# Optimization experiments

Measured on AMD Instinct MI355X. Metric: run time of the kernel, lower is better.

Reference implementation:

```python
import jax, jax.numpy as jnp
import numpy as np

G = 3040      # number of drugs / graph nodes in the drug-drug graph
A = 100       # atoms per molecular graph (smileNode, uniform)
TOK = 43      # token vocabulary (hard-coded in module)
FS = 75       # nfeat_smile
HS = 128      # nhid_smile
H1S = 128     # nhid1_smile
NF = 512      # nfeat (raw 384 + 128 smile emb)
NH = 256      # nhid
DH = 256      # dhid1


def setup_inputs() -> dict:
    key = jax.random.key(0)
    ks = jax.random.split(key, 20)
    s = 0.05
    inp = {
        "x": jax.random.normal(ks[0], (G, NF - H1S), dtype=jnp.float32),
        "adj_pos": jax.random.uniform(ks[1], (G, G), dtype=jnp.float32) / G,
        "adj_neg": jax.random.uniform(ks[2], (G, G), dtype=jnp.float32) / G,
        "mol_adj": jax.random.uniform(ks[3], (G, A, A), dtype=jnp.float32) / A,
        "encoded_drug": jax.random.randint(ks[4], (G, A), 0, TOK, dtype=jnp.int64),
        # learned params
        "tok_emb": jax.random.normal(ks[5], (TOK, FS), dtype=jnp.float32),
        "Wm1": jax.random.normal(ks[6], (G, FS, HS), dtype=jnp.float32) * s,
        "Wm2": jax.random.normal(ks[7], (G, HS, H1S), dtype=jnp.float32) * s,
        "Wp1": jax.random.normal(ks[8], (NF, NH), dtype=jnp.float32) * s,
        "Wp2": jax.random.normal(ks[9], (NH, NH), dtype=jnp.float32) * s,
        "Wn1": jax.random.normal(ks[10], (NF, NH), dtype=jnp.float32) * s,
        "Wn2": jax.random.normal(ks[11], (NH, NH), dtype=jnp.float32) * s,
        "Wd1": jax.random.normal(ks[12], (2 * NH, DH), dtype=jnp.float32) * s,
        "Wd2": jax.random.normal(ks[13], (DH, 2 * DH), dtype=jnp.float32) * s,
        "Wd3": jax.random.normal(ks[14], (2 * DH, DH), dtype=jnp.float32) * s,
        "Wdec": jax.random.normal(ks[15], (DH, DH), dtype=jnp.float32) * s,
    }
    return inp


def reference(x, adj_pos, adj_neg, mol_adj, encoded_drug, tok_emb,
              Wm1, Wm2, Wp1, Wp2, Wn1, Wn2, Wd1, Wd2, Wd3, Wdec):
    # --- calDrugSmileFeatures: batched over all 3040 per-graph GCN encoders ---
    feats = tok_emb[encoded_drug]                          # [G, A, FS] (embedding gather)
    h = jnp.einsum('gab,gaf,gfh->gbh', mol_adj, feats, Wm1)  # gc1: adj @ (x @ W1), per graph
    h = jnp.einsum('gab,gah,ghk->gbk', mol_adj, h, Wm2)      # gc2 (dropout inactive, eval)
    emb_drugs = jnp.max(h, axis=1)                          # [G, H1S] node-wise maxpool

    # --- main drug-drug graph ---
    xc = jnp.concatenate([x, emb_drugs], axis=1)            # [G, NF]
    hp = jax.nn.relu(adj_pos @ (xc @ Wp1))                  # GCNEncoder pos layer1
    zp = adj_pos @ (hp @ Wp2)                               # layer2
    hn = jax.nn.relu(adj_neg @ (xc @ Wn1))
    zn = adj_neg @ (hn @ Wn2)
    z = jnp.concatenate([zp, zn], axis=1)                   # [G, 2*NH]

    # --- DSN MLP (eval: dropout inactive) ---
    z = jax.nn.relu(z @ Wd1)
    z = jax.nn.relu(z @ Wd2)
    z = z @ Wd3                                             # [G, DH]

    # --- Bilinear decoder: z W z^T logits ---
    y_pred = (z @ Wdec) @ z.T                               # [G, G]
    return y_pred
```

## Files before the change

kernel.cpp:

```cpp
#include <hip/hip_runtime.h>
#include <cstdint>
#include <cstddef>

#define Gn   3040
#define An   100
#define TOKn 43
#define FSn  75
#define NFn  512
#define XC   384

typedef __attribute__((ext_vector_type(8))) short s16x8;
typedef __attribute__((ext_vector_type(4))) float f32x4;

__device__ __forceinline__ void split_bf16(float x, unsigned short &h, unsigned short &l)
{
  unsigned u = __float_as_uint(x);
  unsigned r = (u + 0x7fffu + ((u >> 16) & 1u)) & 0xffff0000u;
  h = (unsigned short)(r >> 16);
  float res = x - __uint_as_float(r);
  unsigned v = __float_as_uint(res);
  l = (unsigned short)((v + 0x7fffu + ((v >> 16) & 1u)) >> 16);
}

#define MFMA3(acc, ah, al, bh, bl)                                              \
  acc = __builtin_amdgcn_mfma_f32_16x16x32_bf16(ah, bh, acc, 0, 0, 0);          \
  acc = __builtin_amdgcn_mfma_f32_16x16x32_bf16(ah, bl, acc, 0, 0, 0);          \
  acc = __builtin_amdgcn_mfma_f32_16x16x32_bf16(al, bh, acc, 0, 0, 0);

__device__ __forceinline__ s16x8 tail_frag(const unsigned short* p, bool act)
{
  s16x8 f = {0,0,0,0,0,0,0,0};
  if (act) {
    uint2 v = *(const uint2*)p;
    f[0] = (short)(v.x & 0xffffu); f[1] = (short)(v.x >> 16);
    f[2] = (short)(v.y & 0xffffu); f[3] = (short)(v.y >> 16);
  }
  return f;
}

__device__ __forceinline__ void pack_split4(const f32x4 a, uint2 &ph, uint2 &pl)
{
  unsigned short h[4], l[4];
  #pragma unroll
  for (int r = 0; r < 4; ++r) split_bf16(a[r], h[r], l[r]);
  ph.x = (unsigned)h[0] | ((unsigned)h[1] << 16);
  ph.y = (unsigned)h[2] | ((unsigned)h[3] << 16);
  pl.x = (unsigned)l[0] | ((unsigned)l[1] << 16);
  pl.y = (unsigned)l[2] | ((unsigned)l[3] << 16);
}

__global__ void prep_tok_kernel(const float* __restrict__ tok_emb,
                                unsigned short* __restrict__ th,
                                unsigned short* __restrict__ tl)
{
  int i = blockIdx.x * 256 + threadIdx.x;
  if (i >= TOKn * 96) return;
  int r = i / 96, f = i % 96;
  float v = (f < FSn) ? tok_emb[r * FSn + f] : 0.f;
  unsigned short h, l;
  split_bf16(v, h, l);
  th[i] = h; tl[i] = l;
}

__global__ __launch_bounds__(512, 1) void smile_mfma_kernel(
    const float* __restrict__ mol_adj, const int* __restrict__ enc,
    const unsigned short* __restrict__ tokh, const unsigned short* __restrict__ tokl,
    const float* __restrict__ Wm1, const float* __restrict__ Wm2,
    float* __restrict__ xc)
{
  __shared__ __align__(16) unsigned short sm[74624];
  unsigned short* adjT_h = sm;
  unsigned short* adjT_l = sm + 10400;
  unsigned short* bufA_h = sm + 20800;
  unsigned short* bufA_l = sm + 34112;
  unsigned short* g1_h   = sm + 47424;
  unsigned short* g1_l   = sm + 61024;
  float* Sf = (float*)(sm + 20800);

  const int g = blockIdx.x;
  const int t = threadIdx.x;
  const int w = t >> 6, l = t & 63;
  const int lr = l & 15, lq = l >> 4;
  const f32x4 z4 = {0.f, 0.f, 0.f, 0.f};
  const s16x8 z8 = {0,0,0,0,0,0,0,0};

  const float* adjg = mol_adj + (size_t)g * (An * An);
  float4 av[5];
  #pragma unroll
  for (int j = 0; j < 5; ++j) {
    const int i = t + 512 * j;
    av[j] = make_float4(0.f, 0.f, 0.f, 0.f);
    if (i < 2500) av[j] = *(const float4*)&adjg[i * 4];
  }
  const int hcol = 16 * w + lr;
  const float* W1 = Wm1 + (size_t)g * (FSn * 128);
  float w1r[3][8];
  #pragma unroll
  for (int kc = 0; kc < 3; ++kc)
    #pragma unroll
    for (int j = 0; j < 8; ++j) {
      const int f = 32 * kc + 8 * lq + j;
      w1r[kc][j] = (f < FSn) ? W1[f * 128 + hcol] : 0.f;
    }
  const float* W2 = Wm2 + (size_t)g * (128 * 128);
  float w2r[4][8];
  #pragma unroll
  for (int kc = 0; kc < 4; ++kc)
    #pragma unroll
    for (int j = 0; j < 8; ++j)
      w2r[kc][j] = W2[(32 * kc + 8 * lq + j) * 128 + hcol];
  int tkid[7];
  #pragma unroll
  for (int mi = 0; mi < 7; ++mi) {
    const int a = 16 * mi + lr;
    tkid[mi] = (a < An) ? enc[g * An + a] : 0;
  }

  #pragma unroll
  for (int j = 0; j < 5; ++j) {
    const int i = t + 512 * j;
    if (i < 2500) {
      const int a = i / 25, c4 = (i % 25) * 4;
      float* p = &Sf[a * 101 + c4];
      p[0] = av[j].x; p[1] = av[j].y; p[2] = av[j].z; p[3] = av[j].w;
    }
  }
  __syncthreads();

  #pragma unroll
  for (int j = 0; j < 5; ++j) {
    const int i = t + 512 * j;
    if (i < 2500) {
      const int b = i / 25, a4 = (i % 25) * 4;
      f32x4 v;
      #pragma unroll
      for (int q = 0; q < 4; ++q) v[q] = Sf[(a4 + q) * 101 + b];
      uint2 ph, pl;
      pack_split4(v, ph, pl);
      *(uint2*)&adjT_h[b * 104 + a4] = ph;
      *(uint2*)&adjT_l[b * 104 + a4] = pl;
    }
  }
  __syncthreads();

  {
    s16x8 bh[3], bl[3];
    #pragma unroll
    for (int kc = 0; kc < 3; ++kc)
      #pragma unroll
      for (int j = 0; j < 8; ++j) {
        unsigned short hh, ll;
        split_bf16(w1r[kc][j], hh, ll);
        bh[kc][j] = (short)hh; bl[kc][j] = (short)ll;
      }
    f32x4 acc[7];
    #pragma unroll
    for (int mi = 0; mi < 7; ++mi) acc[mi] = z4;
    #pragma unroll
    for (int mi = 0; mi < 7; ++mi) {
      const unsigned short* th = tokh + tkid[mi] * 96 + 8 * lq;
      const unsigned short* tl = tokl + tkid[mi] * 96 + 8 * lq;
      #pragma unroll
      for (int kc = 0; kc < 3; ++kc) {
        s16x8 ah = *(const s16x8*)&th[32 * kc];
        s16x8 al = *(const s16x8*)&tl[32 * kc];
        MFMA3(acc[mi], ah, al, bh[kc], bl[kc]);
      }
    }
    #pragma unroll
    for (int mi = 0; mi < 7; ++mi) {
      const int a0 = 16 * mi + 4 * lq;
      if (a0 < An) {
        uint2 ph, pl;
        pack_split4(acc[mi], ph, pl);
        *(uint2*)&bufA_h[hcol * 104 + a0] = ph;
        *(uint2*)&bufA_l[hcol * 104 + a0] = pl;
      }
    }
  }
  __syncthreads();

  {
    const unsigned short* xh = &bufA_h[hcol * 104];
    const unsigned short* xl = &bufA_l[hcol * 104];
    f32x4 acc[7];
    #pragma unroll
    for (int ni = 0; ni < 7; ++ni) acc[ni] = z4;
    #pragma unroll
    for (int kc = 0; kc < 4; ++kc) {
      s16x8 ah, al;
      if (kc < 3) {
        ah = *(const s16x8*)&xh[32 * kc + 8 * lq];
        al = *(const s16x8*)&xl[32 * kc + 8 * lq];
      } else {
        ah = tail_frag(xh + 96, lq == 0);
        al = tail_frag(xl + 96, lq == 0);
      }
      #pragma unroll
      for (int ni = 0; ni < 7; ++ni) {
        const int b = 16 * ni + lr;
        const bool vb = b < An;
        s16x8 bh = z8, bl = z8;
        if (kc < 3) {
          if (vb) {
            bh = *(const s16x8*)&adjT_h[b * 104 + 32 * kc + 8 * lq];
            bl = *(const s16x8*)&adjT_l[b * 104 + 32 * kc + 8 * lq];
          }
        } else {
          bh = tail_frag(&adjT_h[b * 104 + 96], vb && lq == 0);
          bl = tail_frag(&adjT_l[b * 104 + 96], vb && lq == 0);
        }
        MFMA3(acc[ni], ah, al, bh, bl);
      }
    }
    __syncthreads();
    #pragma unroll
    for (int ni = 0; ni < 7; ++ni) {
      const int b = 16 * ni + lr;
      if (b < An) {
        uint2 ph, pl;
        pack_split4(acc[ni], ph, pl);
        *(uint2*)&g1_h[b * 136 + 16 * w + 4 * lq] = ph;
        *(uint2*)&g1_l[b * 136 + 16 * w + 4 * lq] = pl;
      }
    }
  }
  __syncthreads();

  {
    s16x8 bh[4], bl[4];
    #pragma unroll
    for (int kc = 0; kc < 4; ++kc)
      #pragma unroll
      for (int j = 0; j < 8; ++j) {
        unsigned short hh, ll;
        split_bf16(w2r[kc][j], hh, ll);
        bh[kc][j] = (short)hh; bl[kc][j] = (short)ll;
      }
    f32x4 acc[7];
    #pragma unroll
    for (int mi = 0; mi < 7; ++mi) acc[mi] = z4;
    #pragma unroll
    for (int kc = 0; kc < 4; ++kc) {
      #pragma unroll
      for (int mi = 0; mi < 7; ++mi) {
        const int b = 16 * mi + lr;
        const bool vb = b < An;
        s16x8 ah = z8, al = z8;
        if (vb) {
          ah = *(const s16x8*)&g1_h[b * 136 + 32 * kc + 8 * lq];
          al = *(const s16x8*)&g1_l[b * 136 + 32 * kc + 8 * lq];
        }
        MFMA3(acc[mi], ah, al, bh[kc], bl[kc]);
      }
    }
    __syncthreads();
    #pragma unroll
    for (int mi = 0; mi < 7; ++mi) {
      const int b0 = 16 * mi + 4 * lq;
      if (b0 < An) {
        uint2 ph, pl;
        pack_split4(acc[mi], ph, pl);
        *(uint2*)&bufA_h[hcol * 104 + b0] = ph;
        *(uint2*)&bufA_l[hcol * 104 + b0] = pl;
      }
    }
  }
  __syncthreads();

  {
    const unsigned short* fh = &bufA_h[hcol * 104];
    const unsigned short* fl = &bufA_l[hcol * 104];
    f32x4 acc[7];
    #pragma unroll
    for (int ni = 0; ni < 7; ++ni) acc[ni] = z4;
    #pragma unroll
    for (int kc = 0; kc < 4; ++kc) {
      s16x8 ah, al;
      if (kc < 3) {
        ah = *(const s16x8*)&fh[32 * kc + 8 * lq];
        al = *(const s16x8*)&fl[32 * kc + 8 * lq];
      } else {
        ah = tail_frag(fh + 96, lq == 0);
        al = tail_frag(fl + 96, lq == 0);
      }
      #pragma unroll
      for (int ni = 0; ni < 7; ++ni) {
        const int b = 16 * ni + lr;
        const bool vb = b < An;
        s16x8 bh = z8, bl = z8;
        if (kc < 3) {
          if (vb) {
            bh = *(const s16x8*)&adjT_h[b * 104 + 32 * kc + 8 * lq];
            bl = *(const s16x8*)&adjT_l[b * 104 + 32 * kc + 8 * lq];
          }
        } else {
          bh = tail_frag(&adjT_h[b * 104 + 96], vb && lq == 0);
          bl = tail_frag(&adjT_l[b * 104 + 96], vb && lq == 0);
        }
        MFMA3(acc[ni], ah, al, bh, bl);
      }
    }
    float mr[4] = {-3.4e38f, -3.4e38f, -3.4e38f, -3.4e38f};
    #pragma unroll
    for (int ni = 0; ni < 7; ++ni) {
      if (16 * ni + lr < An) {
        #pragma unroll
        for (int r = 0; r < 4; ++r) mr[r] = fmaxf(mr[r], acc[ni][r]);
      }
    }
    #pragma unroll
    for (int d = 1; d < 16; d <<= 1) {
      #pragma unroll
      for (int r = 0; r < 4; ++r) mr[r] = fmaxf(mr[r], __shfl_xor(mr[r], d, 64));
    }
    if (lr == 0) {
      const int k2b = 16 * w + 4 * lq;
      #pragma unroll
      for (int r = 0; r < 4; ++r)
        xc[(size_t)g * NFn + XC + k2b + r] = mr[r];
    }
  }
}

__global__ __launch_bounds__(256, 2) void gemm64_kernel(
    const float* __restrict__ A0, const float* __restrict__ A1,
    const float* __restrict__ B0, const float* __restrict__ B1,
    float* __restrict__ C0, float* __restrict__ C1,
    int M, int N, int K, int relu)
{
  const float* A = blockIdx.z ? A1 : A0;
  const float* B = blockIdx.z ? B1 : B0;
  float*       C = blockIdx.z ? C1 : C0;

  __shared__ float As[16][68];
  __shared__ float Bs[16][68];

  const int t  = threadIdx.x;
  const int m0 = blockIdx.x * 64, n0 = blockIdx.y * 64;
  const int tx = t & 15, ty = t >> 4;
  const int am = t >> 2,  ak = (t & 3) * 4;
  const int bk = t >> 4,  bn = (t & 15) * 4;

  float acc[4][4];
  #pragma unroll
  for (int i = 0; i < 4; ++i)
    #pragma unroll
    for (int j = 0; j < 4; ++j) acc[i][j] = 0.f;

  for (int k0 = 0; k0 < K; k0 += 16) {
    float4 av = make_float4(0.f, 0.f, 0.f, 0.f);
    if (m0 + am < M) av = *(const float4*)&A[(size_t)(m0 + am) * K + k0 + ak];
    float4 bv = *(const float4*)&B[(size_t)(k0 + bk) * N + n0 + bn];
    __syncthreads();
    As[ak + 0][am] = av.x; As[ak + 1][am] = av.y;
    As[ak + 2][am] = av.z; As[ak + 3][am] = av.w;
    *(float4*)&Bs[bk][bn] = bv;
    __syncthreads();
    #pragma unroll
    for (int kk = 0; kk < 16; ++kk) {
      float4 a4 = *(const float4*)&As[kk][ty * 4];
      float4 b4 = *(const float4*)&Bs[kk][tx * 4];
      const float aa[4] = {a4.x, a4.y, a4.z, a4.w};
      const float bb[4] = {b4.x, b4.y, b4.z, b4.w};
      #pragma unroll
      for (int i = 0; i < 4; ++i)
        #pragma unroll
        for (int j = 0; j < 4; ++j)
          acc[i][j] = fmaf(aa[i], bb[j], acc[i][j]);
    }
  }
  #pragma unroll
  for (int i = 0; i < 4; ++i) {
    int m = m0 + ty * 4 + i;
    if (m < M) {
      float4 v = make_float4(acc[i][0], acc[i][1], acc[i][2], acc[i][3]);
      if (relu) {
        v.x = fmaxf(v.x, 0.f); v.y = fmaxf(v.y, 0.f);
        v.z = fmaxf(v.z, 0.f); v.w = fmaxf(v.w, 0.f);
      }
      *(float4*)&C[(size_t)m * N + n0 + tx * 4] = v;
    }
  }
}

__global__ __launch_bounds__(256) void convT_kernel(
    const float* __restrict__ S0, const float* __restrict__ S1,
    unsigned short* __restrict__ H0, unsigned short* __restrict__ L0,
    unsigned short* __restrict__ H1, unsigned short* __restrict__ L1)
{
  __shared__ float sT[32][33];
  const float* S     = blockIdx.z ? S1 : S0;
  unsigned short* H  = blockIdx.z ? H1 : H0;
  unsigned short* Lo = blockIdx.z ? L1 : L0;
  const int t  = threadIdx.x;
  const int r0 = blockIdx.x * 32;
  const int c0 = blockIdx.y * 32;
  {
    const int i = t >> 3, j0 = (t & 7) * 4;
    float4 v = *(const float4*)&S[(size_t)(r0 + i) * 256 + c0 + j0];
    sT[i][j0] = v.x; sT[i][j0+1] = v.y; sT[i][j0+2] = v.z; sT[i][j0+3] = v.w;
  }
  __syncthreads();
  {
    const int jj = t >> 3, ii0 = (t & 7) * 4;
    unsigned short h[4], lo[4];
    #pragma unroll
    for (int q = 0; q < 4; ++q) split_bf16(sT[ii0 + q][jj], h[q], lo[q]);
    ushort4 hv = make_ushort4(h[0], h[1], h[2], h[3]);
    ushort4 lv = make_ushort4(lo[0], lo[1], lo[2], lo[3]);
    *(ushort4*)&H [(size_t)(c0 + jj) * Gn + r0 + ii0] = hv;
    *(ushort4*)&Lo[(size_t)(c0 + jj) * Gn + r0 + ii0] = lv;
  }
}

template<bool SPLIT, bool BF32>
__global__ __launch_bounds__(256, 2) void mgemm_kernel(
    const float* __restrict__ A0, const float* __restrict__ A1,
    const unsigned short* __restrict__ Bh0, const unsigned short* __restrict__ Bl0,
    const unsigned short* __restrict__ Bh1, const unsigned short* __restrict__ Bl1,
    const float* __restrict__ Bf,
    float* __restrict__ C0, float* __restrict__ C1,
    int M, int N, int K)
{
  __shared__ __align__(16) unsigned short lds[16384];

  const int z = blockIdx.z;
  int pair, k0base, kend;
  if (SPLIT) {
    pair = z & 1;
    int s = z >> 1;
    k0base = s * 768;
    kend = k0base + 768; if (kend > K) kend = K;
  } else { pair = 0; k0base = 0; kend = K; }

  const float* A = pair ? A1 : A0;
  const unsigned short* Bh = pair ? Bh1 : Bh0;
  const unsigned short* Bl = pair ? Bl1 : Bl0;
  float* C;
  if (SPLIT) C = (pair ? C1 : C0) + (size_t)(z >> 1) * M * N;
  else       C = C0;

  const int t  = threadIdx.x;
  const int l  = t & 63;
  const int wv = t >> 6;
  const int wr = wv >> 1, wc = wv & 1;
  const int m0 = blockIdx.x * 128, n0 = blockIdx.y * 128;

  const int sm = (t >> 6) * 16 + (t & 15);
  const int sk = ((t >> 4) & 3) * 8;

  const f32x4 zero4 = {0.f, 0.f, 0.f, 0.f};
  f32x4 acc[4][4];
  #pragma unroll
  for (int i = 0; i < 4; ++i)
    #pragma unroll
    for (int j = 0; j < 4; ++j) acc[i][j] = zero4;

  for (int k0 = k0base; k0 < kend; k0 += 32) {
    float4 a00 = make_float4(0.f,0.f,0.f,0.f), a01 = a00, a10 = a00, a11 = a00;
    {
      const size_t base = (size_t)(m0 + sm) * K + k0 + sk;
      if (m0 + sm < M)      { a00 = *(const float4*)&A[base];
                              a01 = *(const float4*)&A[base + 4]; }
      if (m0 + sm + 64 < M) { a10 = *(const float4*)&A[base + (size_t)64 * K];
                              a11 = *(const float4*)&A[base + (size_t)64 * K + 4]; }
    }
    s16x8 b0h, b0l, b1h, b1l;
    float4 bf00, bf01, bf10, bf11;
    if (BF32) {
      bf00 = make_float4(0.f,0.f,0.f,0.f); bf01 = bf00; bf10 = bf00; bf11 = bf00;
      const size_t base = (size_t)(n0 + sm) * K + k0 + sk;
      if (n0 + sm < N)      { bf00 = *(const float4*)&Bf[base];
                              bf01 = *(const float4*)&Bf[base + 4]; }
      if (n0 + sm + 64 < N) { bf10 = *(const float4*)&Bf[base + (size_t)64 * K];
                              bf11 = *(const float4*)&Bf[base + (size_t)64 * K + 4]; }
    } else {
      const size_t base = (size_t)(n0 + sm) * K + k0 + sk;
      b0h = *(const s16x8*)&Bh[base];
      b0l = *(const s16x8*)&Bl[base];
      b1h = *(const s16x8*)&Bh[base + (size_t)64 * K];
      b1l = *(const s16x8*)&Bl[base + (size_t)64 * K];
    }

    s16x8 a0h, a0l, a1h, a1l;
    {
      const float av0[8] = {a00.x,a00.y,a00.z,a00.w,a01.x,a01.y,a01.z,a01.w};
      const float av1[8] = {a10.x,a10.y,a10.z,a10.w,a11.x,a11.y,a11.z,a11.w};
      #pragma unroll
      for (int j = 0; j < 8; ++j) {
        unsigned short hh, ll;
        split_bf16(av0[j], hh, ll); a0h[j] = (short)hh; a0l[j] = (short)ll;
        split_bf16(av1[j], hh, ll); a1h[j] = (short)hh; a1l[j] = (short)ll;
      }
    }
    if (BF32) {
      const float bv0[8] = {bf00.x,bf00.y,bf00.z,bf00.w,bf01.x,bf01.y,bf01.z,bf01.w};
      const float bv1[8] = {bf10.x,bf10.y,bf10.z,bf10.w,bf11.x,bf11.y,bf11.z,bf11.w};
      #pragma unroll
      for (int j = 0; j < 8; ++j) {
        unsigned short hh, ll;
        split_bf16(bv0[j], hh, ll); b0h[j] = (short)hh; b0l[j] = (short)ll;
        split_bf16(bv1[j], hh, ll); b1h[j] = (short)hh; b1l[j] = (short)ll;
      }
    }

    __syncthreads();
    {
      const int sl = (t & 63) * 8;
      const int c1 = t >> 6, c2 = c1 + 4;
      *(s16x8*)&lds[c1 * 512 + sl]          = a0h;
      *(s16x8*)&lds[4096 + c1 * 512 + sl]   = a0l;
      *(s16x8*)&lds[c2 * 512 + sl]          = a1h;
      *(s16x8*)&lds[4096 + c2 * 512 + sl]   = a1l;
      *(s16x8*)&lds[8192  + c1 * 512 + sl]  = b0h;
      *(s16x8*)&lds[12288 + c1 * 512 + sl]  = b0l;
      *(s16x8*)&lds[8192  + c2 * 512 + sl]  = b1h;
      *(s16x8*)&lds[12288 + c2 * 512 + sl]  = b1l;
    }
    __syncthreads();

    s16x8 vbh[4], vbl[4];
    #pragma unroll
    for (int ni = 0; ni < 4; ++ni) {
      const int c = wc * 4 + ni;
      vbh[ni] = *(const s16x8*)&lds[8192  + c * 512 + l * 8];
      vbl[ni] = *(const s16x8*)&lds[12288 + c * 512 + l * 8];
    }
    #pragma unroll
    for (int mi = 0; mi < 4; ++mi) {
      const int c = wr * 4 + mi;
      s16x8 ah = *(const s16x8*)&lds[c * 512 + l * 8];
      s16x8 al = *(const s16x8*)&lds[4096 + c * 512 + l * 8];
      #pragma unroll
      for (int ni = 0; ni < 4; ++ni) {
        acc[mi][ni] = __builtin_amdgcn_mfma_f32_16x16x32_bf16(ah, vbh[ni], acc[mi][ni], 0, 0, 0);
        acc[mi][ni] = __builtin_amdgcn_mfma_f32_16x16x32_bf16(ah, vbl[ni], acc[mi][ni], 0, 0, 0);
        acc[mi][ni] = __builtin_amdgcn_mfma_f32_16x16x32_bf16(al, vbh[ni], acc[mi][ni], 0, 0, 0);
      }
    }
  }

  #pragma unroll
  for (int mi = 0; mi < 4; ++mi) {
    const int rowb = m0 + (wr * 4 + mi) * 16 + (l >> 4) * 4;
    #pragma unroll
    for (int ni = 0; ni < 4; ++ni) {
      const int col = n0 + (wc * 4 + ni) * 16 + (l & 15);
      if (col < N) {
        #pragma unroll
        for (int r = 0; r < 4; ++r) {
          const int row = rowb + r;
          if (row < M) C[(size_t)row * N + col] = acc[mi][ni][r];
        }
      }
    }
  }
}

__global__ void reduce_kernel(const float* __restrict__ part, float* __restrict__ dst,
                              int S, int M, int N, int ldc, int coff, int relu)
{
  int i = blockIdx.x * blockDim.x + threadIdx.x;
  int total = M * (N / 4);
  if (i >= total) return;
  int r = i / (N / 4), c = (i % (N / 4)) * 4;
  float4 s = make_float4(0.f, 0.f, 0.f, 0.f);
  for (int j = 0; j < S; ++j) {
    float4 v = *(const float4*)&part[(size_t)j * M * N + (size_t)r * N + c];
    s.x += v.x; s.y += v.y; s.z += v.z; s.w += v.w;
  }
  if (relu) {
    s.x = fmaxf(s.x, 0.f); s.y = fmaxf(s.y, 0.f);
    s.z = fmaxf(s.z, 0.f); s.w = fmaxf(s.w, 0.f);
  }
  *(float4*)&dst[(size_t)r * ldc + coff + c] = s;
}

__global__ void copyx_kernel(const float* __restrict__ x, float* __restrict__ xc)
{
  int i = blockIdx.x * blockDim.x + threadIdx.x;
  int total = Gn * (XC / 4);
  if (i >= total) return;
  int r = i / (XC / 4), c = (i % (XC / 4)) * 4;
  *(float4*)&xc[(size_t)r * NFn + c] = *(const float4*)&x[(size_t)r * XC + c];
}

extern "C" void kernel_launch(void* const* d_in, const int* in_sizes, int n_in,
                              void* d_out, int out_size, void* d_ws, size_t ws_size,
                              hipStream_t stream)
{
  const float* x       = (const float*)d_in[0];
  const float* adj_pos = (const float*)d_in[1];
  const float* adj_neg = (const float*)d_in[2];
  const float* mol_adj = (const float*)d_in[3];
  const int*   enc     = (const int*)d_in[4];
  const float* tok_emb = (const float*)d_in[5];
  const float* Wm1     = (const float*)d_in[6];
  const float* Wm2     = (const float*)d_in[7];
  const float* Wp1     = (const float*)d_in[8];
  const float* Wp2     = (const float*)d_in[9];
  const float* Wn1     = (const float*)d_in[10];
  const float* Wn2     = (const float*)d_in[11];
  const float* Wd1     = (const float*)d_in[12];
  const float* Wd2     = (const float*)d_in[13];
  const float* Wd3     = (const float*)d_in[14];
  const float* Wdec    = (const float*)d_in[15];
  float* out = (float*)d_out;
  float* ws  = (float*)d_ws;

  const size_t MN  = (size_t)Gn * 256;
  const size_t MN2 = (size_t)Gn * 512;
  size_t o = 0;
  float* xc    = ws + o; o += MN2;
  float* P1    = ws + o; o += MN;
  float* N1    = ws + o; o += MN;
  float* hp    = ws + o; o += MN;
  float* hn    = ws + o; o += MN;
  float* P2    = ws + o; o += MN;
  float* N2    = ws + o; o += MN;
  float* zbuf  = ws + o; o += MN2;
  float* d1    = ws + o; o += MN;
  float* d2    = ws + o; o += MN2;
  float* z3    = ws + o; o += MN;
  float* tb    = ws + o; o += MN;
  float* partP = ws + o; o += 4 * MN;
  float* partN = ws + o; o += 4 * MN;
  unsigned short* tokh = (unsigned short*)(ws + o);
  unsigned short* tokl = tokh + TOKn * 96; o += 4128;

  unsigned short* BTPh = (unsigned short*)d2;
  unsigned short* BTPl = BTPh + (size_t)256 * Gn;
  unsigned short* BTNh = BTPh + (size_t)2 * 256 * Gn;
  unsigned short* BTNl = BTPh + (size_t)3 * 256 * Gn;

  dim3 b256(256);

  prep_tok_kernel<<<dim3((TOKn * 96 + 255) / 256), b256, 0, stream>>>(tok_emb, tokh, tokl);
  copyx_kernel<<<dim3((Gn * (XC / 4) + 255) / 256), b256, 0, stream>>>(x, xc);
  smile_mfma_kernel<<<dim3(Gn), dim3(512), 0, stream>>>(
      mol_adj, enc, tokh, tokl, Wm1, Wm2, xc);
  gemm64_kernel<<<dim3(48, 4, 2), b256, 0, stream>>>(xc, xc, Wp1, Wn1, P1, N1, Gn, 256, 512, 0);
  convT_kernel<<<dim3(95, 8, 2), b256, 0, stream>>>(P1, N1, BTPh, BTPl, BTNh, BTNl);
  mgemm_kernel<true, false><<<dim3(24, 2, 8), b256, 0, stream>>>(
      adj_pos, adj_neg, BTPh, BTPl, BTNh, BTNl, (const float*)nullptr,
      partP, partN, Gn, 256, Gn);
  reduce_kernel<<<dim3(760), b256, 0, stream>>>(partP, hp, 4, Gn, 256, 256, 0, 1);
  reduce_kernel<<<dim3(760), b256, 0, stream>>>(partN, hn, 4, Gn, 256, 256, 0, 1);
  gemm64_kernel<<<dim3(48, 4, 2), b256, 0, stream>>>(hp, hn, Wp2, Wn2, P2, N2, Gn, 256, 256, 0);
  convT_kernel<<<dim3(95, 8, 2), b256, 0, stream>>>(P2, N2, BTPh, BTPl, BTNh, BTNl);
  mgemm_kernel<true, false><<<dim3(24, 2, 8), b256, 0, stream>>>(
      adj_pos, adj_neg, BTPh, BTPl, BTNh, BTNl, (const float*)nullptr,
      partP, partN, Gn, 256, Gn);
  reduce_kernel<<<dim3(760), b256, 0, stream>>>(partP, zbuf, 4, Gn, 256, 512, 0, 0);
  reduce_kernel<<<dim3(760), b256, 0, stream>>>(partN, zbuf, 4, Gn, 256, 512, 256, 0);
  gemm64_kernel<<<dim3(48, 4, 1), b256, 0, stream>>>(zbuf, zbuf, Wd1, Wd1, d1, d1, Gn, 256, 512, 1);
  gemm64_kernel<<<dim3(48, 8, 1), b256, 0, stream>>>(d1, d1, Wd2, Wd2, d2, d2, Gn, 512, 256, 1);
  gemm64_kernel<<<dim3(48, 4, 1), b256, 0, stream>>>(d2, d2, Wd3, Wd3, z3, z3, Gn, 256, 512, 0);
  gemm64_kernel<<<dim3(48, 4, 1), b256, 0, stream>>>(z3, z3, Wdec, Wdec, tb, tb, Gn, 256, 256, 0);
  mgemm_kernel<false, true><<<dim3(24, 24, 1), b256, 0, stream>>>(
      tb, tb, (const unsigned short*)nullptr, (const unsigned short*)nullptr,
      (const unsigned short*)nullptr, (const unsigned short*)nullptr,
      z3, out, out, Gn, Gn, 256);
}
```

Measured before the change: 990.2 us.

## Move dense weight GEMMs to split-bf16 MFMA and widen smile kernel to 1024 threads

Replaces the scalar FP32 gemm64 kernel with an MFMA-based wgemm that uses a three-term bf16 hi/lo split. Weights are pre-split and transposed once by a new prep_w kernel, and the wgemm epilogue writes the transposed bf16 hi/lo operands directly, removing the separate convT passes. The per-graph smile kernel now runs with 1024 threads split into two row halves and combines the max-pool through shared memory, so each thread holds fewer registers. This adds a launch and extra workspace, and the split-bf16 arithmetic may lose a little precision compared with plain FP32.

```diff
diff --git a/kernel.cpp b/kernel.cpp
--- a/kernel.cpp
+++ b/kernel.cpp
@@ -62,13 +62,56 @@
   th[i] = h; tl[i] = l;
 }
 
-__global__ __launch_bounds__(512, 1) void smile_mfma_kernel(
+__global__ __launch_bounds__(256) void prep_w_kernel(
+    const float* __restrict__ Wp1, const float* __restrict__ Wn1,
+    const float* __restrict__ Wp2, const float* __restrict__ Wn2,
+    const float* __restrict__ Wd1, const float* __restrict__ Wd2,
+    const float* __restrict__ Wd3, const float* __restrict__ Wdec,
+    unsigned short* __restrict__ WS)
+{
+  __shared__ float sT[32][33];
+  const float* S; int K, N; unsigned off;
+  switch (blockIdx.z) {
+    case 0:  S = Wp1;  K = 512; N = 256; off = 0;       break;
+    case 1:  S = Wn1;  K = 512; N = 256; off = 262144;  break;
+    case 2:  S = Wp2;  K = 256; N = 256; off = 524288;  break;
+    case 3:  S = Wn2;  K = 256; N = 256; off = 655360;  break;
+    case 4:  S = Wd1;  K = 512; N = 256; off = 786432;  break;
+    case 5:  S = Wd2;  K = 256; N = 512; off = 1048576; break;
+    case 6:  S = Wd3;  K = 512; N = 256; off = 1310720; break;
+    default: S = Wdec; K = 256; N = 256; off = 1572864; break;
+  }
+  const int r0 = blockIdx.x * 32, c0 = blockIdx.y * 32;
+  if (r0 >= K || c0 >= N) return;
+  unsigned short* H = WS + off;
+  unsigned short* L = H + K * N;
+  const int t = threadIdx.x;
+  {
+    const int i = t >> 3, j0 = (t & 7) * 4;
+    float4 v = *(const float4*)&S[(size_t)(r0 + i) * N + c0 + j0];
+    sT[i][j0] = v.x; sT[i][j0+1] = v.y; sT[i][j0+2] = v.z; sT[i][j0+3] = v.w;
+  }
+  __syncthreads();
+  {
+    const int jj = t >> 3, ii0 = (t & 7) * 4;
+    unsigned short h[4], lo[4];
+    #pragma unroll
+    for (int q = 0; q < 4; ++q) split_bf16(sT[ii0 + q][jj], h[q], lo[q]);
+    ushort4 hv = make_ushort4(h[0], h[1], h[2], h[3]);
+    ushort4 lv = make_ushort4(lo[0], lo[1], lo[2], lo[3]);
+    *(ushort4*)&H[(size_t)(c0 + jj) * K + r0 + ii0] = hv;
+    *(ushort4*)&L[(size_t)(c0 + jj) * K + r0 + ii0] = lv;
+  }
+}
+
+__global__ __launch_bounds__(1024, 1) void smile_mfma_kernel(
     const float* __restrict__ mol_adj, const int* __restrict__ enc,
     const unsigned short* __restrict__ tokh, const unsigned short* __restrict__ tokl,
     const float* __restrict__ Wm1, const float* __restrict__ Wm2,
     float* __restrict__ xc)
 {
   __shared__ __align__(16) unsigned short sm[74624];
+  __shared__ float sMax[8][2][16];
   unsigned short* adjT_h = sm;
   unsigned short* adjT_l = sm + 10400;
   unsigned short* bufA_h = sm + 20800;
@@ -80,56 +123,29 @@
   const int g = blockIdx.x;
   const int t = threadIdx.x;
   const int w = t >> 6, l = t & 63;
+  const int wc = w & 7, wr = w >> 3;
   const int lr = l & 15, lq = l >> 4;
+  const int hcol = 16 * wc + lr;
+  const int NI = wr ? 3 : 4;
+  const int IB = wr * 4;
   const f32x4 z4 = {0.f, 0.f, 0.f, 0.f};
   const s16x8 z8 = {0,0,0,0,0,0,0,0};
 
   const float* adjg = mol_adj + (size_t)g * (An * An);
-  float4 av[5];
   #pragma unroll
-  for (int j = 0; j < 5; ++j) {
-    const int i = t + 512 * j;
-    av[j] = make_float4(0.f, 0.f, 0.f, 0.f);
-    if (i < 2500) av[j] = *(const float4*)&adjg[i * 4];
-  }
-  const int hcol = 16 * w + lr;
-  const float* W1 = Wm1 + (size_t)g * (FSn * 128);
-  float w1r[3][8];
-  #pragma unroll
-  for (int kc = 0; kc < 3; ++kc)
-    #pragma unroll
-    for (int j = 0; j < 8; ++j) {
-      const int f = 32 * kc + 8 * lq + j;
-      w1r[kc][j] = (f < FSn) ? W1[f * 128 + hcol] : 0.f;
-    }
-  const float* W2 = Wm2 + (size_t)g * (128 * 128);
-  float w2r[4][8];
-  #pragma unroll
-  for (int kc = 0; kc < 4; ++kc)
-    #pragma unroll
-    for (int j = 0; j < 8; ++j)
-      w2r[kc][j] = W2[(32 * kc + 8 * lq + j) * 128 + hcol];
-  int tkid[7];
-  #pragma unroll
-  for (int mi = 0; mi < 7; ++mi) {
-    const int a = 16 * mi + lr;
-    tkid[mi] = (a < An) ? enc[g * An + a] : 0;
-  }
-
-  #pragma unroll
-  for (int j = 0; j < 5; ++j) {
-    const int i = t + 512 * j;
+  for (int j = 0; j < 3; ++j) {
+    const int i = t + 1024 * j;
     if (i < 2500) {
+      float4 v = *(const float4*)&adjg[i * 4];
       const int a = i / 25, c4 = (i % 25) * 4;
       float* p = &Sf[a * 101 + c4];
-      p[0] = av[j].x; p[1] = av[j].y; p[2] = av[j].z; p[3] = av[j].w;
+      p[0] = v.x; p[1] = v.y; p[2] = v.z; p[3] = v.w;
     }
   }
   __syncthreads();
-
   #pragma unroll
-  for (int j = 0; j < 5; ++j) {
-    const int i = t + 512 * j;
+  for (int j = 0; j < 3; ++j) {
+    const int i = t + 1024 * j;
     if (i < 2500) {
       const int b = i / 25, a4 = (i % 25) * 4;
       f32x4 v;
@@ -144,37 +160,48 @@
   __syncthreads();
 
   {
+    const float* W1 = Wm1 + (size_t)g * (FSn * 128);
     s16x8 bh[3], bl[3];
     #pragma unroll
     for (int kc = 0; kc < 3; ++kc)
       #pragma unroll
       for (int j = 0; j < 8; ++j) {
+        const int f = 32 * kc + 8 * lq + j;
+        float v = (f < FSn) ? W1[f * 128 + hcol] : 0.f;
         unsigned short hh, ll;
-        split_bf16(w1r[kc][j], hh, ll);
+        split_bf16(v, hh, ll);
         bh[kc][j] = (short)hh; bl[kc][j] = (short)ll;
       }
-    f32x4 acc[7];
-    #pragma unroll
-    for (int mi = 0; mi < 7; ++mi) acc[mi] = z4;
-    #pragma unroll
-    for (int mi = 0; mi < 7; ++mi) {
-      const unsigned short* th = tokh + tkid[mi] * 96 + 8 * lq;
-      const unsigned short* tl = tokl + tkid[mi] * 96 + 8 * lq;
-      #pragma unroll
-      for (int kc = 0; kc < 3; ++kc) {
-        s16x8 ah = *(const s16x8*)&th[32 * kc];
-        s16x8 al = *(const s16x8*)&tl[32 * kc];
-        MFMA3(acc[mi], ah, al, bh[kc], bl[kc]);
-      }
-    }
-    #pragma unroll
-    for (int mi = 0; mi < 7; ++mi) {
-      const int a0 = 16 * mi + 4 * lq;
-      if (a0 < An) {
-        uint2 ph, pl;
-        pack_split4(acc[mi], ph, pl);
-        *(uint2*)&bufA_h[hcol * 104 + a0] = ph;
-        *(uint2*)&bufA_l[hcol * 104 + a0] = pl;
+    f32x4 acc[4];
+    #pragma unroll
+    for (int i = 0; i < 4; ++i) acc[i] = z4;
+    #pragma unroll
+    for (int m2 = 0; m2 < 4; ++m2) {
+      if (m2 < NI) {
+        const int mi = IB + m2;
+        const int a = 16 * mi + lr;
+        const bool va = a < An;
+        const int tk = va ? enc[g * An + a] : 0;
+        const unsigned short* th = tokh + tk * 96 + 8 * lq;
+        const unsigned short* tl = tokl + tk * 96 + 8 * lq;
+        #pragma unroll
+        for (int kc = 0; kc < 3; ++kc) {
+          s16x8 ah = z8, al = z8;
+          if (va) { ah = *(const s16x8*)&th[32 * kc]; al = *(const s16x8*)&tl[32 * kc]; }
+          MFMA3(acc[m2], ah, al, bh[kc], bl[kc]);
+        }
+      }
+    }
+    #pragma unroll
+    for (int m2 = 0; m2 < 4; ++m2) {
+      if (m2 < NI) {
+        const int a0 = 16 * (IB + m2) + 4 * lq;
+        if (a0 < An) {
+          uint2 ph, pl;
+          pack_split4(acc[m2], ph, pl);
+          *(uint2*)&bufA_h[hcol * 104 + a0] = ph;
+          *(uint2*)&bufA_l[hcol * 104 + a0] = pl;
+        }
       }
     }
   }
@@ -183,9 +210,9 @@
   {
     const unsigned short* xh = &bufA_h[hcol * 104];
     const unsigned short* xl = &bufA_l[hcol * 104];
-    f32x4 acc[7];
-    #pragma unroll
-    for (int ni = 0; ni < 7; ++ni) acc[ni] = z4;
+    f32x4 acc[4];
+    #pragma unroll
+    for (int i = 0; i < 4; ++i) acc[i] = z4;
     #pragma unroll
     for (int kc = 0; kc < 4; ++kc) {
       s16x8 ah, al;
@@ -197,72 +224,79 @@
         al = tail_frag(xl + 96, lq == 0);
       }
       #pragma unroll
-      for (int ni = 0; ni < 7; ++ni) {
-        const int b = 16 * ni + lr;
-        const bool vb = b < An;
-        s16x8 bh = z8, bl = z8;
-        if (kc < 3) {
-          if (vb) {
-            bh = *(const s16x8*)&adjT_h[b * 104 + 32 * kc + 8 * lq];
-            bl = *(const s16x8*)&adjT_l[b * 104 + 32 * kc + 8 * lq];
+      for (int n2 = 0; n2 < 4; ++n2) {
+        if (n2 < NI) {
+          const int b = 16 * (IB + n2) + lr;
+          const bool vb = b < An;
+          s16x8 bh = z8, bl = z8;
+          if (kc < 3) {
+            if (vb) {
+              bh = *(const s16x8*)&adjT_h[b * 104 + 32 * kc + 8 * lq];
+              bl = *(const s16x8*)&adjT_l[b * 104 + 32 * kc + 8 * lq];
+            }
+          } else {
+            bh = tail_frag(&adjT_h[b * 104 + 96], vb && lq == 0);
+            bl = tail_frag(&adjT_l[b * 104 + 96], vb && lq == 0);
           }
-        } else {
-          bh = tail_frag(&adjT_h[b * 104 + 96], vb && lq == 0);
-          bl = tail_frag(&adjT_l[b * 104 + 96], vb && lq == 0);
-        }
-        MFMA3(acc[ni], ah, al, bh, bl);
-      }
-    }
-    __syncthreads();
-    #pragma unroll
-    for (int ni = 0; ni < 7; ++ni) {
-      const int b = 16 * ni + lr;
-      if (b < An) {
-        uint2 ph, pl;
-        pack_split4(acc[ni], ph, pl);
-        *(uint2*)&g1_h[b * 136 + 16 * w + 4 * lq] = ph;
-        *(uint2*)&g1_l[b * 136 + 16 * w + 4 * lq] = pl;
+          MFMA3(acc[n2], ah, al, bh, bl);
+        }
+      }
+    }
+    #pragma unroll
+    for (int n2 = 0; n2 < 4; ++n2) {
+      if (n2 < NI) {
+        const int b = 16 * (IB + n2) + lr;
+        if (b < An) {
+          uint2 ph, pl;
+          pack_split4(acc[n2], ph, pl);
+          *(uint2*)&g1_h[b * 136 + 16 * wc + 4 * lq] = ph;
+          *(uint2*)&g1_l[b * 136 + 16 * wc + 4 * lq] = pl;
+        }
       }
     }
   }
   __syncthreads();
 
   {
+    const float* W2 = Wm2 + (size_t)g * (128 * 128);
     s16x8 bh[4], bl[4];
     #pragma unroll
     for (int kc = 0; kc < 4; ++kc)
       #pragma unroll
       for (int j = 0; j < 8; ++j) {
         unsigned short hh, ll;
-        split_bf16(w2r[kc][j], hh, ll);
+        split_bf16(W2[(32 * kc + 8 * lq + j) * 128 + hcol], hh, ll);
         bh[kc][j] = (short)hh; bl[kc][j] = (short)ll;
       }
-    f32x4 acc[7];
-    #pragma unroll
-    for (int mi = 0; mi < 7; ++mi) acc[mi] = z4;
+    f32x4 acc[4];
+    #pragma unroll
+    for (int i = 0; i < 4; ++i) acc[i] = z4;
     #pragma unroll
     for (int kc = 0; kc < 4; ++kc) {
       #pragma unroll
-      for (int mi = 0; mi < 7; ++mi) {
-        const int b = 16 * mi + lr;
-        const bool vb = b < An;
-        s16x8 ah = z8, al = z8;
-        if (vb) {
-          ah = *(const s16x8*)&g1_h[b * 136 + 32 * kc + 8 * lq];
-          al = *(const s16x8*)&g1_l[b * 136 + 32 * kc + 8 * lq];
-        }
-        MFMA3(acc[mi], ah, al, bh[kc], bl[kc]);
-      }
-    }
-    __syncthreads();
-    #pragma unroll
-    for (int mi = 0; mi < 7; ++mi) {
-      const int b0 = 16 * mi + 4 * lq;
-      if (b0 < An) {
-        uint2 ph, pl;
-        pack_split4(acc[mi], ph, pl);
-        *(uint2*)&bufA_h[hcol * 104 + b0] = ph;
-        *(uint2*)&bufA_l[hcol * 104 + b0] = pl;
+      for (int m2 = 0; m2 < 4; ++m2) {
+        if (m2 < NI) {
+          const int b = 16 * (IB + m2) + lr;
+          const bool vb = b < An;
+          s16x8 ah = z8, al = z8;
+          if (vb) {
+            ah = *(const s16x8*)&g1_h[b * 136 + 32 * kc + 8 * lq];
+            al = *(const s16x8*)&g1_l[b * 136 + 32 * kc + 8 * lq];
+          }
+          MFMA3(acc[m2], ah, al, bh[kc], bl[kc]);
+        }
+      }
+    }
+    #pragma unroll
+    for (int m2 = 0; m2 < 4; ++m2) {
+      if (m2 < NI) {
+        const int b0 = 16 * (IB + m2) + 4 * lq;
+        if (b0 < An) {
+          uint2 ph, pl;
+          pack_split4(acc[m2], ph, pl);
+          *(uint2*)&bufA_h[hcol * 104 + b0] = ph;
+          *(uint2*)&bufA_l[hcol * 104 + b0] = pl;
+        }
       }
     }
   }
@@ -271,9 +305,9 @@
   {
     const unsigned short* fh = &bufA_h[hcol * 104];
     const unsigned short* fl = &bufA_l[hcol * 104];
-    f32x4 acc[7];
-    #pragma unroll
-    for (int ni = 0; ni < 7; ++ni) acc[ni] = z4;
+    f32x4 acc[4];
+    #pragma unroll
+    for (int i = 0; i < 4; ++i) acc[i] = z4;
     #pragma unroll
     for (int kc = 0; kc < 4; ++kc) {
       s16x8 ah, al;
@@ -285,28 +319,30 @@
         al = tail_frag(fl + 96, lq == 0);
       }
       #pragma unroll
-      for (int ni = 0; ni < 7; ++ni) {
-        const int b = 16 * ni + lr;
-        const bool vb = b < An;
-        s16x8 bh = z8, bl = z8;
-        if (kc < 3) {
-          if (vb) {
-            bh = *(const s16x8*)&adjT_h[b * 104 + 32 * kc + 8 * lq];
-            bl = *(const s16x8*)&adjT_l[b * 104 + 32 * kc + 8 * lq];
+      for (int n2 = 0; n2 < 4; ++n2) {
+        if (n2 < NI) {
+          const int b = 16 * (IB + n2) + lr;
+          const bool vb = b < An;
+          s16x8 bh = z8, bl = z8;
+          if (kc < 3) {
+            if (vb) {
+              bh = *(const s16x8*)&adjT_h[b * 104 + 32 * kc + 8 * lq];
+              bl = *(const s16x8*)&adjT_l[b * 104 + 32 * kc + 8 * lq];
+            }
+          } else {
+            bh = tail_frag(&adjT_h[b * 104 + 96], vb && lq == 0);
+            bl = tail_frag(&adjT_l[b * 104 + 96], vb && lq == 0);
           }
-        } else {
-          bh = tail_frag(&adjT_h[b * 104 + 96], vb && lq == 0);
-          bl = tail_frag(&adjT_l[b * 104 + 96], vb && lq == 0);
-        }
-        MFMA3(acc[ni], ah, al, bh, bl);
+          MFMA3(acc[n2], ah, al, bh, bl);
+        }
       }
     }
     float mr[4] = {-3.4e38f, -3.4e38f, -3.4e38f, -3.4e38f};
     #pragma unroll
-    for (int ni = 0; ni < 7; ++ni) {
-      if (16 * ni + lr < An) {
+    for (int n2 = 0; n2 < 4; ++n2) {
+      if (n2 < NI && (16 * (IB + n2) + lr) < An) {
         #pragma unroll
-        for (int r = 0; r < 4; ++r) mr[r] = fmaxf(mr[r], acc[ni][r]);
+        for (int r = 0; r < 4; ++r) mr[r] = fmaxf(mr[r], acc[n2][r]);
       }
     }
     #pragma unroll
@@ -315,102 +351,18 @@
       for (int r = 0; r < 4; ++r) mr[r] = fmaxf(mr[r], __shfl_xor(mr[r], d, 64));
     }
     if (lr == 0) {
-      const int k2b = 16 * w + 4 * lq;
-      #pragma unroll
-      for (int r = 0; r < 4; ++r)
-        xc[(size_t)g * NFn + XC + k2b + r] = mr[r];
-    }
-  }
-}
-
-__global__ __launch_bounds__(256, 2) void gemm64_kernel(
-    const float* __restrict__ A0, const float* __restrict__ A1,
-    const float* __restrict__ B0, const float* __restrict__ B1,
-    float* __restrict__ C0, float* __restrict__ C1,
-    int M, int N, int K, int relu)
-{
-  const float* A = blockIdx.z ? A1 : A0;
-  const float* B = blockIdx.z ? B1 : B0;
-  float*       C = blockIdx.z ? C1 : C0;
-
-  __shared__ float As[16][68];
-  __shared__ float Bs[16][68];
-
-  const int t  = threadIdx.x;
-  const int m0 = blockIdx.x * 64, n0 = blockIdx.y * 64;
-  const int tx = t & 15, ty = t >> 4;
-  const int am = t >> 2,  ak = (t & 3) * 4;
-  const int bk = t >> 4,  bn = (t & 15) * 4;
-
-  float acc[4][4];
-  #pragma unroll
-  for (int i = 0; i < 4; ++i)
-    #pragma unroll
-    for (int j = 0; j < 4; ++j) acc[i][j] = 0.f;
-
-  for (int k0 = 0; k0 < K; k0 += 16) {
-    float4 av = make_float4(0.f, 0.f, 0.f, 0.f);
-    if (m0 + am < M) av = *(const float4*)&A[(size_t)(m0 + am) * K + k0 + ak];
-    float4 bv = *(const float4*)&B[(size_t)(k0 + bk) * N + n0 + bn];
-    __syncthreads();
-    As[ak + 0][am] = av.x; As[ak + 1][am] = av.y;
-    As[ak + 2][am] = av.z; As[ak + 3][am] = av.w;
-    *(float4*)&Bs[bk][bn] = bv;
-    __syncthreads();
-    #pragma unroll
-    for (int kk = 0; kk < 16; ++kk) {
-      float4 a4 = *(const float4*)&As[kk][ty * 4];
-      float4 b4 = *(const float4*)&Bs[kk][tx * 4];
-      const float aa[4] = {a4.x, a4.y, a4.z, a4.w};
-      const float bb[4] = {b4.x, b4.y, b4.z, b4.w};
-      #pragma unroll
-      for (int i = 0; i < 4; ++i)
-        #pragma unroll
-        for (int j = 0; j < 4; ++j)
-          acc[i][j] = fmaf(aa[i], bb[j], acc[i][j]);
-    }
-  }
-  #pragma unroll
-  for (int i = 0; i < 4; ++i) {
-    int m = m0 + ty * 4 + i;
-    if (m < M) {
-      float4 v = make_float4(acc[i][0], acc[i][1], acc[i][2], acc[i][3]);
-      if (relu) {
-        v.x = fmaxf(v.x, 0.f); v.y = fmaxf(v.y, 0.f);
-        v.z = fmaxf(v.z, 0.f); v.w = fmaxf(v.w, 0.f);
-      }
-      *(float4*)&C[(size_t)m * N + n0 + tx * 4] = v;
-    }
-  }
-}
-
-__global__ __launch_bounds__(256) void convT_kernel(
-    const float* __restrict__ S0, const float* __restrict__ S1,
-    unsigned short* __restrict__ H0, unsigned short* __restrict__ L0,
-    unsigned short* __restrict__ H1, unsigned short* __restrict__ L1)
-{
-  __shared__ float sT[32][33];
-  const float* S     = blockIdx.z ? S1 : S0;
-  unsigned short* H  = blockIdx.z ? H1 : H0;
-  unsigned short* Lo = blockIdx.z ? L1 : L0;
-  const int t  = threadIdx.x;
-  const int r0 = blockIdx.x * 32;
-  const int c0 = blockIdx.y * 32;
-  {
-    const int i = t >> 3, j0 = (t & 7) * 4;
-    float4 v = *(const float4*)&S[(size_t)(r0 + i) * 256 + c0 + j0];
-    sT[i][j0] = v.x; sT[i][j0+1] = v.y; sT[i][j0+2] = v.z; sT[i][j0+3] = v.w;
+      #pragma unroll
+      for (int r = 0; r < 4; ++r) sMax[wc][wr][4 * lq + r] = mr[r];
+    }
   }
   __syncthreads();
-  {
-    const int jj = t >> 3, ii0 = (t & 7) * 4;
-    unsigned short h[4], lo[4];
-    #pragma unroll
-    for (int q = 0; q < 4; ++q) split_bf16(sT[ii0 + q][jj], h[q], lo[q]);
-    ushort4 hv = make_ushort4(h[0], h[1], h[2], h[3]);
-    ushort4 lv = make_ushort4(lo[0], lo[1], lo[2], lo[3]);
-    *(ushort4*)&H [(size_t)(c0 + jj) * Gn + r0 + ii0] = hv;
-    *(ushort4*)&Lo[(size_t)(c0 + jj) * Gn + r0 + ii0] = lv;
+  if (wr == 0 && lr == 0) {
+    #pragma unroll
+    for (int r = 0; r < 4; ++r) {
+      const int h = 16 * wc + 4 * lq + r;
+      xc[(size_t)g * NFn + XC + h] =
+          fmaxf(sMax[wc][0][4 * lq + r], sMax[wc][1][4 * lq + r]);
+    }
   }
 }
 
@@ -552,6 +504,147 @@
         for (int r = 0; r < 4; ++r) {
           const int row = rowb + r;
           if (row < M) C[(size_t)row * N + col] = acc[mi][ni][r];
+        }
+      }
+    }
+  }
+}
+
+template<int EOUT>
+__global__ __launch_bounds__(256, 2) void wgemm_kernel(
+    const float* __restrict__ A0, const float* __restrict__ A1,
+    const unsigned short* __restrict__ Bh0, const unsigned short* __restrict__ Bl0,
+    const unsigned short* __restrict__ Bh1, const unsigned short* __restrict__ Bl1,
+    float* __restrict__ C0, float* __restrict__ C1,
+    unsigned short* __restrict__ H0, unsigned short* __restrict__ L0,
+    unsigned short* __restrict__ H1, unsigned short* __restrict__ L1,
+    int M, int N, int K)
+{
+  __shared__ __align__(16) unsigned short lds[16384];
+
+  const int pair = blockIdx.z;
+  const float* A = pair ? A1 : A0;
+  const unsigned short* Bh = pair ? Bh1 : Bh0;
+  const unsigned short* Bl = pair ? Bl1 : Bl0;
+
+  const int t  = threadIdx.x;
+  const int l  = t & 63;
+  const int wv = t >> 6;
+  const int wr = wv >> 1, wc = wv & 1;
+  const int m0 = blockIdx.x * 128, n0 = blockIdx.y * 128;
+
+  const int sm = (t >> 6) * 16 + (t & 15);
+  const int sk = ((t >> 4) & 3) * 8;
+
+  const f32x4 zero4 = {0.f, 0.f, 0.f, 0.f};
+  f32x4 acc[4][4];
+  #pragma unroll
+  for (int i = 0; i < 4; ++i)
+    #pragma unroll
+    for (int j = 0; j < 4; ++j) acc[i][j] = zero4;
+
+  for (int k0 = 0; k0 < K; k0 += 32) {
+    float4 a00 = make_float4(0.f,0.f,0.f,0.f), a01 = a00, a10 = a00, a11 = a00;
+    {
+      const size_t base = (size_t)(m0 + sm) * K + k0 + sk;
+      if (m0 + sm < M)      { a00 = *(const float4*)&A[base];
+                              a01 = *(const float4*)&A[base + 4]; }
+      if (m0 + sm + 64 < M) { a10 = *(const float4*)&A[base + (size_t)64 * K];
+                              a11 = *(const float4*)&A[base + (size_t)64 * K + 4]; }
+    }
+    s16x8 b0h, b0l, b1h, b1l;
+    {
+      const size_t base = (size_t)(n0 + sm) * K + k0 + sk;
+      b0h = *(const s16x8*)&Bh[base];
+      b0l = *(const s16x8*)&Bl[base];
+      b1h = *(const s16x8*)&Bh[base + (size_t)64 * K];
+      b1l = *(const s16x8*)&Bl[base + (size_t)64 * K];
+    }
+    s16x8 a0h, a0l, a1h, a1l;
+    {
+      const float av0[8] = {a00.x,a00.y,a00.z,a00.w,a01.x,a01.y,a01.z,a01.w};
+      const float av1[8] = {a10.x,a10.y,a10.z,a10.w,a11.x,a11.y,a11.z,a11.w};
+      #pragma unroll
+      for (int j = 0; j < 8; ++j) {
+        unsigned short hh, ll;
+        split_bf16(av0[j], hh, ll); a0h[j] = (short)hh; a0l[j] = (short)ll;
+        split_bf16(av1[j], hh, ll); a1h[j] = (short)hh; a1l[j] = (short)ll;
+      }
+    }
+
+    __syncthreads();
+    {
+      const int sl = (t & 63) * 8;
+      const int c1 = t >> 6, c2 = c1 + 4;
+      *(s16x8*)&lds[c1 * 512 + sl]          = a0h;
+      *(s16x8*)&lds[4096 + c1 * 512 + sl]   = a0l;
+      *(s16x8*)&lds[c2 * 512 + sl]          = a1h;
+      *(s16x8*)&lds[4096 + c2 * 512 + sl]   = a1l;
+      *(s16x8*)&lds[8192  + c1 * 512 + sl]  = b0h;
+      *(s16x8*)&lds[12288 + c1 * 512 + sl]  = b0l;
+      *(s16x8*)&lds[8192  + c2 * 512 + sl]  = b1h;
+      *(s16x8*)&lds[12288 + c2 * 512 + sl]  = b1l;
+    }
+    __syncthreads();
+
+    s16x8 vbh[4], vbl[4];
+    #pragma unroll
+    for (int ni = 0; ni < 4; ++ni) {
+      const int c = wc * 4 + ni;
+      vbh[ni] = *(const s16x8*)&lds[8192  + c * 512 + l * 8];
+      vbl[ni] = *(const s16x8*)&lds[12288 + c * 512 + l * 8];
+    }
+    #pragma unroll
+    for (int mi = 0; mi < 4; ++mi) {
+      const int c = wr * 4 + mi;
+      s16x8 ah = *(const s16x8*)&lds[c * 512 + l * 8];
+      s16x8 al = *(const s16x8*)&lds[4096 + c * 512 + l * 8];
+      #pragma unroll
+      for (int ni = 0; ni < 4; ++ni) {
+        acc[mi][ni] = __builtin_amdgcn_mfma_f32_16x16x32_bf16(ah, vbh[ni], acc[mi][ni], 0, 0, 0);
+        acc[mi][ni] = __builtin_amdgcn_mfma_f32_16x16x32_bf16(ah, vbl[ni], acc[mi][ni], 0, 0, 0);
+        acc[mi][ni] = __builtin_amdgcn_mfma_f32_16x16x32_bf16(al, vbh[ni], acc[mi][ni], 0, 0, 0);
+      }
+    }
+  }
+
+  if (EOUT <= 1) {
+    float* C = pair ? C1 : C0;
+    #pragma unroll
+    for (int mi = 0; mi < 4; ++mi) {
+      const int rowb = m0 + (wr * 4 + mi) * 16 + (l >> 4) * 4;
+      #pragma unroll
+      for (int ni = 0; ni < 4; ++ni) {
+        const int col = n0 + (wc * 4 + ni) * 16 + (l & 15);
+        if (col < N) {
+          #pragma unroll
+          for (int r = 0; r < 4; ++r) {
+            const int row = rowb + r;
+            if (row < M) {
+              float v = acc[mi][ni][r];
+              if (EOUT == 1) v = fmaxf(v, 0.f);
+              C[(size_t)row * N + col] = v;
+            }
+          }
+        }
+      }
+    }
+  } else {
+    unsigned short* H = pair ? H1 : H0;
+    unsigned short* L = pair ? L1 : L0;
+    #pragma unroll
+    for (int mi = 0; mi < 4; ++mi) {
+      const int rowb = m0 + (wr * 4 + mi) * 16 + (l >> 4) * 4;
+      if (rowb < M) {
+        #pragma unroll
+        for (int ni = 0; ni < 4; ++ni) {
+          const int col = n0 + (wc * 4 + ni) * 16 + (l & 15);
+          if (col < N) {
+            uint2 ph, pl;
+            pack_split4(acc[mi][ni], ph, pl);
+            *(uint2*)&H[(size_t)col * M + rowb] = ph;
+            *(uint2*)&L[(size_t)col * M + rowb] = pl;
+          }
         }
       }
     }
@@ -628,6 +721,15 @@
   float* partN = ws + o; o += 4 * MN;
   unsigned short* tokh = (unsigned short*)(ws + o);
   unsigned short* tokl = tokh + TOKn * 96; o += 4128;
+  unsigned short* WS = (unsigned short*)(ws + o); o += 851968;
+  unsigned short* Wp1s  = WS + 0;
+  unsigned short* Wn1s  = WS + 262144;
+  unsigned short* Wp2s  = WS + 524288;
+  unsigned short* Wn2s  = WS + 655360;
+  unsigned short* Wd1s  = WS + 786432;
+  unsigned short* Wd2s  = WS + 1048576;
+  unsigned short* Wd3s  = WS + 1310720;
+  unsigned short* Wdecs = WS + 1572864;
 
   unsigned short* BTPh = (unsigned short*)d2;
   unsigned short* BTPl = BTPh + (size_t)256 * Gn;
@@ -637,27 +739,39 @@
   dim3 b256(256);
 
   prep_tok_kernel<<<dim3((TOKn * 96 + 255) / 256), b256, 0, stream>>>(tok_emb, tokh, tokl);
+  prep_w_kernel<<<dim3(16, 16, 8), b256, 0, stream>>>(
+      Wp1, Wn1, Wp2, Wn2, Wd1, Wd2, Wd3, Wdec, WS);
   copyx_kernel<<<dim3((Gn * (XC / 4) + 255) / 256), b256, 0, stream>>>(x, xc);
-  smile_mfma_kernel<<<dim3(Gn), dim3(512), 0, stream>>>(
+  smile_mfma_kernel<<<dim3(Gn), dim3(1024), 0, stream>>>(
       mol_adj, enc, tokh, tokl, Wm1, Wm2, xc);
-  gemm64_kernel<<<dim3(48, 4, 2), b256, 0, stream>>>(xc, xc, Wp1, Wn1, P1, N1, Gn, 256, 512, 0);
-  convT_kernel<<<dim3(95, 8, 2), b256, 0, stream>>>(P1, N1, BTPh, BTPl, BTNh, BTNl);
+  wgemm_kernel<2><<<dim3(24, 2, 2), b256, 0, stream>>>(
+      xc, xc, Wp1s, Wp1s + 131072, Wn1s, Wn1s + 131072,
+      nullptr, nullptr, BTPh, BTPl, BTNh, BTNl, Gn, 256, 512);
   mgemm_kernel<true, false><<<dim3(24, 2, 8), b256, 0, stream>>>(
       adj_pos, adj_neg, BTPh, BTPl, BTNh, BTNl, (const float*)nullptr,
       partP, partN, Gn, 256, Gn);
   reduce_kernel<<<dim3(760), b256, 0, stream>>>(partP, hp, 4, Gn, 256, 256, 0, 1);
   reduce_kernel<<<dim3(760), b256, 0, stream>>>(partN, hn, 4, Gn, 256, 256, 0, 1);
-  gemm64_kernel<<<dim3(48, 4, 2), b256, 0, stream>>>(hp, hn, Wp2, Wn2, P2, N2, Gn, 256, 256, 0);
-  convT_kernel<<<dim3(95, 8, 2), b256, 0, stream>>>(P2, N2, BTPh, BTPl, BTNh, BTNl);
+  wgemm_kernel<2><<<dim3(24, 2, 2), b256, 0, stream>>>(
+      hp, hn, Wp2s, Wp2s + 65536, Wn2s, Wn2s + 65536,
+      nullptr, nullptr, BTPh, BTPl, BTNh, BTNl, Gn, 256, 256);
   mgemm_kernel<true, false><<<dim3(24, 2, 8), b256, 0, stream>>>(
       adj_pos, adj_neg, BTPh, BTPl, BTNh, BTNl, (const float*)nullptr,
       partP, partN, Gn, 256, Gn);
   reduce_kernel<<<dim3(760), b256, 0, stream>>>(partP, zbuf, 4, Gn, 256, 512, 0, 0);
   reduce_kernel<<<dim3(760), b256, 0, stream>>>(partN, zbuf, 4, Gn, 256, 512, 256, 0);
-  gemm64_kernel<<<dim3(48, 4, 1), b256, 0, stream>>>(zbuf, zbuf, Wd1, Wd1, d1, d1, Gn, 256, 512, 1);
-  gemm64_kernel<<<dim3(48, 8, 1), b256, 0, stream>>>(d1, d1, Wd2, Wd2, d2, d2, Gn, 512, 256, 1);
-  gemm64_kernel<<<dim3(48, 4, 1), b256, 0, stream>>>(d2, d2, Wd3, Wd3, z3, z3, Gn, 256, 512, 0);
-  gemm64_kernel<<<dim3(48, 4, 1), b256, 0, stream>>>(z3, z3, Wdec, Wdec, tb, tb, Gn, 256, 256, 0);
+  wgemm_kernel<1><<<dim3(24, 2, 1), b256, 0, stream>>>(
+      zbuf, zbuf, Wd1s, Wd1s + 131072, Wd1s, Wd1s + 131072,
+      d1, d1, nullptr, nullptr, nullptr, nullptr, Gn, 256, 512);
+  wgemm_kernel<1><<<dim3(24, 4, 1), b256, 0, stream>>>(
+      d1, d1, Wd2s, Wd2s + 131072, Wd2s, Wd2s + 131072,
+      d2, d2, nullptr, nullptr, nullptr, nullptr, Gn, 512, 256);
+  wgemm_kernel<0><<<dim3(24, 2, 1), b256, 0, stream>>>(
+      d2, d2, Wd3s, Wd3s + 131072, Wd3s, Wd3s + 131072,
+      z3, z3, nullptr, nullptr, nullptr, nullptr, Gn, 256, 512);
+  wgemm_kernel<0><<<dim3(24, 2, 1), b256, 0, stream>>>(
+      z3, z3, Wdecs, Wdecs + 65536, Wdecs, Wdecs + 65536,
+      tb, tb, nullptr, nullptr, nullptr, nullptr, Gn, 256, 256);
   mgemm_kernel<false, true><<<dim3(24, 24, 1), b256, 0, stream>>>(
       tb, tb, (const unsigned short*)nullptr, (const unsigned short*)nullptr,
       (const unsigned short*)nullptr, (const unsigned short*)nullptr,
```

Result: faster. 966.1 us (-2.4%).
